# Performance work log

Hardware: AMD Instinct MI355X
Metric: run time of the kernel (lower is better)

Reference implementation:

```python
import jax, jax.numpy as jnp
import numpy as np

B, S, D, FF, V, H, M = 4, 512, 768, 3072, 30000, 12, 64
DH = D // H
N_LAYERS = 12  # shared ALBERT layer applied 12 times


def _positional_encoding():
    pos = jnp.arange(S, dtype=jnp.float32)[:, None]                      # [S,1]
    denom = jnp.power(10000.0, 2.0 * jnp.arange(D, dtype=jnp.float32) / D)
    pe = pos / denom                                                     # [S,D]
    pe = pe.at[1:, 0::2].set(jnp.sin(pe[1:, 0::2]))
    pe = pe.at[1:, 1::2].set(jnp.cos(pe[1:, 1::2]))
    return pe


def setup_inputs() -> dict:
    key = jax.random.key(0)
    ks = jax.random.split(key, 20)
    tok = jax.random.randint(ks[0], (B, S), 0, V)
    texts_onehot = jax.nn.one_hot(tok, V, dtype=jnp.float32)
    w = lambda k, shp: (jax.random.normal(k, shp, jnp.float32) * 0.02)
    return {
        'texts_onehot': texts_onehot,
        'se_w': w(ks[1], (V, D)), 'se_b': w(ks[2], (D,)),
        'wq': w(ks[3], (D, D)), 'bq': w(ks[4], (D,)),
        'wk': w(ks[5], (D, D)), 'bk': w(ks[6], (D,)),
        'wv': w(ks[7], (D, D)), 'bv': w(ks[8], (D,)),
        'wo': w(ks[9], (D, D)), 'bo': w(ks[10], (D,)),
        'w1': w(ks[11], (D, FF)), 'b1': w(ks[12], (FF,)),
        'w2': w(ks[13], (FF, D)), 'b2': w(ks[14], (D,)),
        'we': w(ks[15], (D, V)), 'be': w(ks[16], (V,)),
        'idx': jax.random.randint(ks[17], (B, M), 0, S),
    }


def _layernorm(x):
    mean = jnp.mean(x, axis=-1, keepdims=True)
    var = jnp.mean(jnp.square(x - mean), axis=-1, keepdims=True)
    return (x - mean) / jnp.sqrt(var + 1e-5)


def reference(texts_onehot, se_w, se_b, wq, bq, wk, bk, wv, bv, wo, bo,
              w1, b1, w2, b2, we, be, idx):
    pe = _positional_encoding()                                          # [S,D]
    x = texts_onehot @ se_w + se_b + pe                                  # [B,S,D]
    scale = 1.0 / jnp.sqrt(jnp.float32(DH))

    def mha(x):
        q = (x @ wq + bq).reshape(B, S, H, DH)
        k = (x @ wk + bk).reshape(B, S, H, DH)
        v = (x @ wv + bv).reshape(B, S, H, DH)
        att = jax.nn.softmax(jnp.einsum('bqhd,bkhd->bhqk', q, k) * scale, axis=-1)
        o = jnp.einsum('bhqk,bkhd->bqhd', att, v).reshape(B, S, D)
        return o @ wo + bo

    for _ in range(N_LAYERS):  # same (shared) weights every iteration
        x = _layernorm(x + mha(x))
        x = jax.nn.relu(x @ w1 + b1) @ w2 + b2

    # gather masked positions then project to vocab + log_softmax
    g = jnp.take_along_axis(x, idx[..., None], axis=1)                   # [B,M,D]
    logits = g @ we + be                                                 # [B,M,V]
    return jax.nn.log_softmax(logits, axis=-1).reshape(B * M, V)
```

## Files before the change

### kernel.cpp

```cpp
#include <hip/hip_runtime.h>
#include <hip/hip_bf16.h>
#include <math.h>

#define Bv 4
#define Sv 512
#define Dv 768
#define FFv 3072
#define Vv 30000
#define Vpad 30080
#define Hv 12
#define Mv 64
#define DHv 64
#define NLAYERS 12
#define QKVN 2304

typedef __attribute__((ext_vector_type(8))) short short8;
typedef __attribute__((ext_vector_type(4))) float floatx4;

static __device__ __forceinline__ short f2b(float f) {
  union { float f; unsigned u; } v; v.f = f;
  unsigned r = v.u + 0x7fffu + ((v.u >> 16) & 1u);
  return (short)(r >> 16);
}

#define GLD16(gp, lp) __builtin_amdgcn_global_load_lds( \
    (__attribute__((address_space(1))) void*)(gp), \
    (__attribute__((address_space(3))) void*)(lp), 16, 0, 0)

__global__ __launch_bounds__(256) void transpose_w(
    const float* __restrict__ W, short* __restrict__ Wt,
    int K, int N, int Nout)
{
  __shared__ float t[32][33];
  int n0 = blockIdx.x * 32, k0 = blockIdx.y * 32;
  int tx = threadIdx.x & 31, ty = threadIdx.x >> 5;
  #pragma unroll
  for (int i = 0; i < 4; i++) {
    int k = k0 + ty + i * 8, n = n0 + tx;
    t[ty + i * 8][tx] = (n < N) ? W[(size_t)k * N + n] : 0.f;
  }
  __syncthreads();
  #pragma unroll
  for (int i = 0; i < 4; i++) {
    int n = n0 + ty + i * 8, k = k0 + tx;
    if (n < Nout) Wt[(size_t)n * K + k] = f2b(t[tx][ty + i * 8]);
  }
}

__global__ __launch_bounds__(256) void pack_bias(
    const float* __restrict__ bq, const float* __restrict__ bk,
    const float* __restrict__ bv, float* __restrict__ bqkv)
{
  int i = blockIdx.x * 256 + threadIdx.x;
  if (i < Dv) { bqkv[i] = bq[i]; bqkv[Dv + i] = bk[i]; bqkv[2 * Dv + i] = bv[i]; }
}

__global__ __launch_bounds__(256) void embed_kernel(
    const float* __restrict__ oh, const float* __restrict__ sew,
    const float* __restrict__ seb, float* __restrict__ xf,
    short* __restrict__ xb)
{
  int bs = blockIdx.x;
  int s = bs & (Sv - 1);
  __shared__ int tokS;
  const float* row = oh + (size_t)bs * Vv;
  for (int j = threadIdx.x * 4; j < Vv; j += 256 * 4) {
    float4 f = *(const float4*)(row + j);
    if (f.x != 0.f) tokS = j;
    if (f.y != 0.f) tokS = j + 1;
    if (f.z != 0.f) tokS = j + 2;
    if (f.w != 0.f) tokS = j + 3;
  }
  __syncthreads();
  int tok = tokS;
  for (int d = threadIdx.x; d < Dv; d += 256) {
    float pe = 0.f;
    if (s > 0) {
      float denom = expf(9.210340371976184f * (2.f * (float)d / 768.f));
      float raw = (float)s / denom;
      pe = (d & 1) ? cosf(raw) : sinf(raw);
    }
    float val = sew[(size_t)tok * Dv + d] + seb[d] + pe;
    xf[(size_t)bs * Dv + d] = val;
    xb[(size_t)bs * Dv + d] = f2b(val);
  }
}

template <int BM, int BN, int WM, int WN, int BK>
__global__ __launch_bounds__(256) void gemm_bt(
    const short* __restrict__ A, const short* __restrict__ Bt,
    const float* __restrict__ bias, float* __restrict__ Cf,
    short* __restrict__ Cb, int M, int N, int K, int relu)
{
  constexpr int CPR = BK / 8;
  constexpr int ITA = BM * BK / 2048;
  constexpr int ITB = BN * BK / 2048;
  constexpr int ITMAX = ITA > ITB ? ITA : ITB;
  __shared__ __align__(16) short As[BM * BK];
  __shared__ __align__(16) short Bs[BN * BK];

  int nwgx = gridDim.x;
  int nwg = nwgx * gridDim.y;
  int fid = blockIdx.y * nwgx + blockIdx.x;
  if ((nwg & 7) == 0) fid = (fid & 7) * (nwg >> 3) + (fid >> 3);
  int n0 = (fid % nwgx) * BN, m0 = (fid / nwgx) * BM;

  int tid = threadIdx.x;
  int wave = tid >> 6, lane = tid & 63, quad = lane >> 4, l16 = lane & 15;
  int wm = (wave >> 1) * WM, wn = (wave & 1) * WN;

  floatx4 acc[WM / 16][WN / 16];
  #pragma unroll
  for (int i = 0; i < WM / 16; i++)
    #pragma unroll
    for (int j = 0; j < WN / 16; j++) acc[i][j] = (floatx4){0.f, 0.f, 0.f, 0.f};

  int srow[ITMAX], skc[ITMAX];
  #pragma unroll
  for (int it = 0; it < ITMAX; it++) {
    int c = it * 256 + tid;
    srow[it] = c / CPR;
    skc[it] = (c & (CPR - 1)) ^ (srow[it] & 7);
  }

  for (int k0 = 0; k0 < K; k0 += BK) {
    __syncthreads();
    #pragma unroll
    for (int it = 0; it < ITA; it++)
      GLD16(A + (size_t)(m0 + srow[it]) * K + k0 + skc[it] * 8,
            As + (it * 2048 + wave * 512));
    #pragma unroll
    for (int it = 0; it < ITB; it++)
      GLD16(Bt + (size_t)(n0 + srow[it]) * K + k0 + skc[it] * 8,
            Bs + (it * 2048 + wave * 512));
    __syncthreads();
    #pragma unroll
    for (int kh = 0; kh < BK / 32; kh++) {
      short8 af[WM / 16], bfr[WN / 16];
      int kc = kh * 4 + quad;
      #pragma unroll
      for (int i = 0; i < WM / 16; i++) {
        int ra = wm + i * 16 + l16;
        af[i] = *(const short8*)(As + (ra * CPR + (kc ^ (ra & 7))) * 8);
      }
      #pragma unroll
      for (int j = 0; j < WN / 16; j++) {
        int rb = wn + j * 16 + l16;
        bfr[j] = *(const short8*)(Bs + (rb * CPR + (kc ^ (rb & 7))) * 8);
      }
      #pragma unroll
      for (int i = 0; i < WM / 16; i++)
        #pragma unroll
        for (int j = 0; j < WN / 16; j++)
          acc[i][j] = __builtin_amdgcn_mfma_f32_16x16x32_bf16(af[i], bfr[j], acc[i][j], 0, 0, 0);
    }
  }

  #pragma unroll
  for (int i = 0; i < WM / 16; i++) {
    int row = m0 + wm + i * 16 + quad * 4;
    #pragma unroll
    for (int j = 0; j < WN / 16; j++) {
      int col = n0 + wn + j * 16 + l16;
      if (col < N) {
        float bb = bias ? bias[col] : 0.f;
        #pragma unroll
        for (int r = 0; r < 4; r++) {
          float val = acc[i][j][r] + bb;
          if (relu) val = fmaxf(val, 0.f);
          size_t off = (size_t)(row + r) * N + col;
          if (Cf) Cf[off] = val;
          if (Cb) Cb[off] = f2b(val);
        }
      }
    }
  }
}

__global__ __launch_bounds__(256) void attn_fused(
    const short* __restrict__ qkv, short* __restrict__ O)
{
  __shared__ __align__(16) short lv[64 * 512];
  __shared__ __align__(16) short pbuf[4][16][40];

  int fid = blockIdx.y * gridDim.x + blockIdx.x;
  fid = (fid & 7) * 48 + (fid >> 3);
  int q0 = (fid & 7) * 64;
  int bh = fid >> 3;
  int b = bh / Hv, h = bh - b * Hv;
  int tid = threadIdx.x;
  int wave = tid >> 6, lane = tid & 63, quad = lane >> 4, l16 = lane & 15;

  floatx4 acc[32];
  #pragma unroll
  for (int c = 0; c < 32; c++) acc[c] = (floatx4){0.f, 0.f, 0.f, 0.f};

  const short* Qrow = qkv + (size_t)(b * Sv + q0 + wave * 16 + l16) * QKVN + h * DHv;
  short8 a0 = *(const short8*)(Qrow + quad * 8);
  short8 a1 = *(const short8*)(Qrow + 32 + quad * 8);
  const short* Kbase = qkv + Dv + (size_t)(b * Sv + l16) * QKVN + h * DHv + quad * 8;
  const short* Vbase = qkv + 2 * Dv + h * DHv + (size_t)(b * Sv) * QKVN;

  int kb_t = tid >> 5;
  int n2_t = (tid & 31) * 2;
  short2 vreg[16];

#define LOADQ(qi) do { \
    _Pragma("unroll") \
    for (int i = 0; i < 16; i++) { \
      int kk = (qi) * 128 + i * 8 + kb_t; \
      vreg[i] = *(const short2*)(Vbase + (size_t)kk * QKVN + n2_t); \
    } } while (0)
#define WRITEQ(qi) do { \
    _Pragma("unroll") \
    for (int i = 0; i < 16; i++) { \
      int ch = (qi) * 16 + i; \
      int sw0 = (ch & ~7) | ((ch ^ n2_t) & 7); \
      lv[n2_t * 512 + sw0 * 8 + kb_t] = vreg[i].x; \
      lv[(n2_t + 1) * 512 + (sw0 ^ 1) * 8 + kb_t] = vreg[i].y; \
    } } while (0)

  #pragma unroll
  for (int g = 0; g < 4; g++) {
    if (g > 0) WRITEQ(g - 1);
    LOADQ(g);
    #pragma unroll
    for (int cc = 0; cc < 8; cc++) {
      int c = g * 8 + cc;
      const short* Kp = Kbase + (size_t)c * 16 * QKVN;
      short8 b0 = *(const short8*)(Kp);
      short8 b1 = *(const short8*)(Kp + 32);
      acc[c] = __builtin_amdgcn_mfma_f32_16x16x32_bf16(a0, b0, acc[c], 0, 0, 0);
      acc[c] = __builtin_amdgcn_mfma_f32_16x16x32_bf16(a1, b1, acc[c], 0, 0, 0);
    }
  }

  float inv[4];
  #pragma unroll
  for (int r = 0; r < 4; r++) {
    float m = -1e30f;
    #pragma unroll
    for (int c = 0; c < 32; c++) m = fmaxf(m, acc[c][r]);
    m = fmaxf(m, __shfl_xor(m, 1));
    m = fmaxf(m, __shfl_xor(m, 2));
    m = fmaxf(m, __shfl_xor(m, 4));
    m = fmaxf(m, __shfl_xor(m, 8));
    float s = 0.f;
    #pragma unroll
    for (int c = 0; c < 32; c++) {
      float e = __expf((acc[c][r] - m) * 0.125f);
      acc[c][r] = e; s += e;
    }
    s += __shfl_xor(s, 1);
    s += __shfl_xor(s, 2);
    s += __shfl_xor(s, 4);
    s += __shfl_xor(s, 8);
    inv[r] = 1.f / s;
  }

  WRITEQ(3);
  __syncthreads();

  floatx4 acc_o[4];
  #pragma unroll
  for (int j = 0; j < 4; j++) acc_o[j] = (floatx4){0.f, 0.f, 0.f, 0.f};

  #pragma unroll
  for (int kc = 0; kc < 16; kc++) {
    #pragma unroll
    for (int half = 0; half < 2; half++) {
      int c = 2 * kc + half;
      #pragma unroll
      for (int r = 0; r < 4; r++)
        pbuf[wave][quad * 4 + r][half * 16 + l16] = f2b(acc[c][r] * inv[r]);
    }
    short8 af = *(const short8*)(&pbuf[wave][l16][quad * 8]);
    #pragma unroll
    for (int j = 0; j < 4; j++) {
      int n = j * 16 + l16;
      int ch = kc * 4 + quad;
      int sw = (ch & ~7) | ((ch ^ n) & 7);
      short8 bf = *(const short8*)(lv + n * 512 + sw * 8);
      acc_o[j] = __builtin_amdgcn_mfma_f32_16x16x32_bf16(af, bf, acc_o[j], 0, 0, 0);
    }
  }
#undef LOADQ
#undef WRITEQ

  int row = q0 + wave * 16 + quad * 4;
  #pragma unroll
  for (int j = 0; j < 4; j++) {
    int col = h * DHv + j * 16 + l16;
    #pragma unroll
    for (int r = 0; r < 4; r++)
      O[(size_t)(b * Sv + row + r) * Dv + col] = f2b(acc_o[j][r]);
  }
}

__global__ __launch_bounds__(256) void addln_kernel(
    float* __restrict__ xf, const float* __restrict__ mh,
    short* __restrict__ xb)
{
  int r = blockIdx.x, t = threadIdx.x;
  size_t base = (size_t)r * Dv;
  float v[3];
  #pragma unroll
  for (int i = 0; i < 3; i++) {
    int d = t + i * 256;
    v[i] = xf[base + d] + mh[base + d];
  }
  __shared__ float red[256];
  red[t] = v[0] + v[1] + v[2];
  __syncthreads();
  for (int s2 = 128; s2 > 0; s2 >>= 1) { if (t < s2) red[t] += red[t + s2]; __syncthreads(); }
  float mean = red[0] * (1.f / 768.f);
  __syncthreads();
  float sq = 0.f;
  #pragma unroll
  for (int i = 0; i < 3; i++) { float d2 = v[i] - mean; sq += d2 * d2; }
  red[t] = sq;
  __syncthreads();
  for (int s2 = 128; s2 > 0; s2 >>= 1) { if (t < s2) red[t] += red[t + s2]; __syncthreads(); }
  float inv = rsqrtf(red[0] * (1.f / 768.f) + 1e-5f);
  #pragma unroll
  for (int i = 0; i < 3; i++) {
    int d = t + i * 256;
    float o = (v[i] - mean) * inv;
    xf[base + d] = o;
    xb[base + d] = f2b(o);
  }
}

__global__ __launch_bounds__(256) void gather_kernel(
    const short* __restrict__ xb, const int* __restrict__ idx,
    short* __restrict__ g)
{
  int bm = blockIdx.x;
  int b = bm >> 6;
  int s = idx[bm];
  for (int d = threadIdx.x; d < Dv; d += 256)
    g[(size_t)bm * Dv + d] = xb[(size_t)(b * Sv + s) * Dv + d];
}

__global__ __launch_bounds__(256) void lsm_kernel(
    const float* __restrict__ L, float* __restrict__ out)
{
  int r = blockIdx.x, t = threadIdx.x;
  const float* p = L + (size_t)r * Vv;
  float m = -1e30f;
  for (int j = t; j < Vv; j += 256) m = fmaxf(m, p[j]);
  __shared__ float red[256];
  red[t] = m;
  __syncthreads();
  for (int s2 = 128; s2 > 0; s2 >>= 1) { if (t < s2) red[t] = fmaxf(red[t], red[t + s2]); __syncthreads(); }
  m = red[0];
  __syncthreads();
  float s = 0.f;
  for (int j = t; j < Vv; j += 256) s += expf(p[j] - m);
  red[t] = s;
  __syncthreads();
  for (int s2 = 128; s2 > 0; s2 >>= 1) { if (t < s2) red[t] += red[t + s2]; __syncthreads(); }
  float lse = m + logf(red[0]);
  for (int j = t; j < Vv; j += 256) out[(size_t)r * Vv + j] = p[j] - lse;
}

extern "C" void kernel_launch(void* const* d_in, const int* in_sizes, int n_in,
                              void* d_out, int out_size, void* d_ws, size_t ws_size,
                              hipStream_t stream) {
  const float* oh  = (const float*)d_in[0];
  const float* sew = (const float*)d_in[1];
  const float* seb = (const float*)d_in[2];
  const float* wq  = (const float*)d_in[3];  const float* bq = (const float*)d_in[4];
  const float* wk  = (const float*)d_in[5];  const float* bk = (const float*)d_in[6];
  const float* wv  = (const float*)d_in[7];  const float* bv = (const float*)d_in[8];
  const float* wo  = (const float*)d_in[9];  const float* bo = (const float*)d_in[10];
  const float* w1  = (const float*)d_in[11]; const float* b1 = (const float*)d_in[12];
  const float* w2  = (const float*)d_in[13]; const float* b2 = (const float*)d_in[14];
  const float* we  = (const float*)d_in[15]; const float* be = (const float*)d_in[16];
  const int*   idx = (const int*)d_in[17];
  float* out = (float*)d_out;

  char* p = (char*)d_ws;
  auto alloc = [&](size_t bytes) -> char* {
    char* r = p; p += (bytes + 255) & ~(size_t)255; return r;
  };
  const size_t BS = (size_t)Bv * Sv;
  short* wqkv_t = (short*)alloc((size_t)QKVN * Dv * 2);
  short* wo_t   = (short*)alloc((size_t)Dv * Dv * 2);
  short* w1_t   = (short*)alloc((size_t)FFv * Dv * 2);
  short* w2_t   = (short*)alloc((size_t)Dv * FFv * 2);
  float* bqkv   = (float*)alloc(QKVN * 4);
  short* xb     = (short*)alloc(BS * Dv * 2);
  float* xf     = (float*)alloc(BS * Dv * 4);
  short* g      = (short*)alloc((size_t)Bv * Mv * Dv * 2);
  char*  TR     = p;
  short* qkv   = (short*)TR;
  short* o     = (short*)(TR + ((BS * QKVN * 2 + 255) & ~(size_t)255));
  float* mh    = (float*)((char*)o + ((BS * Dv * 2 + 255) & ~(size_t)255));
  short* t1    = (short*)((char*)mh + ((BS * Dv * 4 + 255) & ~(size_t)255));
  short* we_t = (short*)TR;
  float* lg   = (float*)(TR + (((size_t)Vpad * Dv * 2 + 255) & ~(size_t)255));

  transpose_w<<<dim3(24, 24), 256, 0, stream>>>(wq, wqkv_t,            Dv, Dv, Dv);
  transpose_w<<<dim3(24, 24), 256, 0, stream>>>(wk, wqkv_t + Dv * Dv,  Dv, Dv, Dv);
  transpose_w<<<dim3(24, 24), 256, 0, stream>>>(wv, wqkv_t + 2*Dv*Dv,  Dv, Dv, Dv);
  transpose_w<<<dim3(24, 24), 256, 0, stream>>>(wo, wo_t,              Dv, Dv, Dv);
  transpose_w<<<dim3(96, 24), 256, 0, stream>>>(w1, w1_t,              Dv, FFv, FFv);
  transpose_w<<<dim3(24, 96), 256, 0, stream>>>(w2, w2_t,              FFv, Dv, Dv);
  pack_bias<<<3, 256, 0, stream>>>(bq, bk, bv, bqkv);

  embed_kernel<<<(int)BS, 256, 0, stream>>>(oh, sew, seb, xf, xb);

  dim3 gQKV(QKVN / 128, (int)BS / 128);
  dim3 gD64(Dv / 64, (int)BS / 64);
  dim3 gFF(FFv / 128, (int)BS / 128);
  for (int l = 0; l < NLAYERS; l++) {
    gemm_bt<128,128,64,64,64><<<gQKV, 256, 0, stream>>>(xb, wqkv_t, bqkv, nullptr, qkv, (int)BS, QKVN, Dv, 0);
    attn_fused<<<dim3(Sv / 64, Bv * Hv), 256, 0, stream>>>(qkv, o);
    gemm_bt<64,64,32,32,128><<<gD64, 256, 0, stream>>>(o, wo_t, bo, mh, nullptr, (int)BS, Dv, Dv, 0);
    addln_kernel<<<(int)BS, 256, 0, stream>>>(xf, mh, xb);
    gemm_bt<128,128,64,64,64><<<gFF, 256, 0, stream>>>(xb, w1_t, b1, nullptr, t1, (int)BS, FFv, Dv, 1);
    gemm_bt<64,64,32,32,128><<<gD64, 256, 0, stream>>>(t1, w2_t, b2, xf, xb, (int)BS, Dv, FFv, 0);
  }

  transpose_w<<<dim3(940, 24), 256, 0, stream>>>(we, we_t, Dv, Vv, Vpad);
  gather_kernel<<<Bv * Mv, 256, 0, stream>>>(xb, idx, g);
  gemm_bt<128,128,64,64,64><<<dim3(Vpad / 128, (Bv * Mv) / 128), 256, 0, stream>>>(
      g, we_t, be, lg, nullptr, Bv * Mv, Vv, Dv, 0);
  lsm_kernel<<<Bv * Mv, 256, 0, stream>>>(lg, out);
}
```

Baseline: 2.055 ms.

## Double-buffer GEMM tiles, fuse vocab weight conversion, and vectorize LN/log-softmax

The bf16 GEMM now double-buffers its LDS tiles, so the global-to-LDS copy of the next K tile runs while MFMAs consume the current one, with a vmcnt wait plus barrier between steps. The vocab projection no longer transposes the 30000x768 fp32 weight up front. A new GEMM reads the fp32 weight directly and converts it to bf16 into LDS on the fly. Add+LayerNorm switches to one wave per row with float4 loads and shuffle reductions, and log-softmax uses float4 accesses. The cost is double the LDS in the GEMM, which may lower occupancy, and scalar 2-byte LDS stores in the new vocab GEMM.

```diff
diff --git a/kernel.cpp b/kernel.cpp
--- a/kernel.cpp
+++ b/kernel.cpp
@@ -15,6 +15,7 @@
 #define QKVN 2304
 
 typedef __attribute__((ext_vector_type(8))) short short8;
+typedef __attribute__((ext_vector_type(4))) short short4v;
 typedef __attribute__((ext_vector_type(4))) float floatx4;
 
 static __device__ __forceinline__ short f2b(float f) {
@@ -26,6 +27,11 @@
 #define GLD16(gp, lp) __builtin_amdgcn_global_load_lds( \
     (__attribute__((address_space(1))) void*)(gp), \
     (__attribute__((address_space(3))) void*)(lp), 16, 0, 0)
+
+#define VMCNT0_BARRIER() do { \
+    asm volatile("s_waitcnt vmcnt(0)" ::: "memory"); \
+    __builtin_amdgcn_s_barrier(); \
+  } while (0)
 
 __global__ __launch_bounds__(256) void transpose_w(
     const float* __restrict__ W, short* __restrict__ Wt,
@@ -96,8 +102,8 @@
   constexpr int ITA = BM * BK / 2048;
   constexpr int ITB = BN * BK / 2048;
   constexpr int ITMAX = ITA > ITB ? ITA : ITB;
-  __shared__ __align__(16) short As[BM * BK];
-  __shared__ __align__(16) short Bs[BN * BK];
+  __shared__ __align__(16) short As[2][BM * BK];
+  __shared__ __align__(16) short Bs[2][BN * BK];
 
   int nwgx = gridDim.x;
   int nwg = nwgx * gridDim.y;
@@ -123,17 +129,23 @@
     skc[it] = (c & (CPR - 1)) ^ (srow[it] & 7);
   }
 
-  for (int k0 = 0; k0 < K; k0 += BK) {
-    __syncthreads();
+  auto stage = [&](int buf, int k0) {
     #pragma unroll
     for (int it = 0; it < ITA; it++)
       GLD16(A + (size_t)(m0 + srow[it]) * K + k0 + skc[it] * 8,
-            As + (it * 2048 + wave * 512));
+            &As[buf][it * 2048 + wave * 512]);
     #pragma unroll
     for (int it = 0; it < ITB; it++)
       GLD16(Bt + (size_t)(n0 + srow[it]) * K + k0 + skc[it] * 8,
-            Bs + (it * 2048 + wave * 512));
-    __syncthreads();
+            &Bs[buf][it * 2048 + wave * 512]);
+  };
+
+  int nt = K / BK;
+  stage(0, 0);
+  VMCNT0_BARRIER();
+  int cur = 0;
+  for (int t = 0; t < nt; t++) {
+    if (t + 1 < nt) stage(cur ^ 1, (t + 1) * BK);
     #pragma unroll
     for (int kh = 0; kh < BK / 32; kh++) {
       short8 af[WM / 16], bfr[WN / 16];
@@ -141,12 +153,12 @@
       #pragma unroll
       for (int i = 0; i < WM / 16; i++) {
         int ra = wm + i * 16 + l16;
-        af[i] = *(const short8*)(As + (ra * CPR + (kc ^ (ra & 7))) * 8);
+        af[i] = *(const short8*)(&As[cur][(ra * CPR + (kc ^ (ra & 7))) * 8]);
       }
       #pragma unroll
       for (int j = 0; j < WN / 16; j++) {
         int rb = wn + j * 16 + l16;
-        bfr[j] = *(const short8*)(Bs + (rb * CPR + (kc ^ (rb & 7))) * 8);
+        bfr[j] = *(const short8*)(&Bs[cur][(rb * CPR + (kc ^ (rb & 7))) * 8]);
       }
       #pragma unroll
       for (int i = 0; i < WM / 16; i++)
@@ -154,6 +166,8 @@
         for (int j = 0; j < WN / 16; j++)
           acc[i][j] = __builtin_amdgcn_mfma_f32_16x16x32_bf16(af[i], bfr[j], acc[i][j], 0, 0, 0);
     }
+    VMCNT0_BARRIER();
+    cur ^= 1;
   }
 
   #pragma unroll
@@ -172,6 +186,97 @@
           if (Cf) Cf[off] = val;
           if (Cb) Cb[off] = f2b(val);
         }
+      }
+    }
+  }
+}
+
+__global__ __launch_bounds__(256) void gemm_bf32(
+    const short* __restrict__ A, const float* __restrict__ B,
+    const float* __restrict__ bias, float* __restrict__ Cf,
+    int M, int N, int K)
+{
+  __shared__ __align__(16) short As[128 * 64];
+  __shared__ __align__(16) short Bs[128 * 64];
+  int n0 = blockIdx.x * 128, m0 = blockIdx.y * 128;
+  int tid = threadIdx.x;
+  int wave = tid >> 6, lane = tid & 63, quad = lane >> 4, l16 = lane & 15;
+  int wm = (wave >> 1) * 64, wn = (wave & 1) * 64;
+
+  floatx4 acc[4][4];
+  #pragma unroll
+  for (int i = 0; i < 4; i++)
+    #pragma unroll
+    for (int j = 0; j < 4; j++) acc[i][j] = (floatx4){0.f, 0.f, 0.f, 0.f};
+
+  int srow[4], skc[4];
+  #pragma unroll
+  for (int it = 0; it < 4; it++) {
+    int c = it * 256 + tid;
+    srow[it] = c >> 3;
+    skc[it] = (c & 7) ^ (srow[it] & 7);
+  }
+  int bk0 = tid >> 5;
+  int bn  = (tid & 31) * 4;
+
+  for (int k0 = 0; k0 < K; k0 += 64) {
+    __syncthreads();
+    #pragma unroll
+    for (int it = 0; it < 4; it++)
+      GLD16(A + (size_t)(m0 + srow[it]) * K + k0 + skc[it] * 8,
+            As + (it * 2048 + wave * 512));
+    #pragma unroll
+    for (int i = 0; i < 8; i++) {
+      int kk = k0 + bk0 + i * 8;
+      int ng = n0 + bn;
+      float4 bv;
+      if (ng + 3 < N) bv = *(const float4*)(B + (size_t)kk * N + ng);
+      else {
+        bv.x = (ng     < N) ? B[(size_t)kk * N + ng]     : 0.f;
+        bv.y = (ng + 1 < N) ? B[(size_t)kk * N + ng + 1] : 0.f;
+        bv.z = (ng + 2 < N) ? B[(size_t)kk * N + ng + 2] : 0.f;
+        bv.w = (ng + 3 < N) ? B[(size_t)kk * N + ng + 3] : 0.f;
+      }
+      int nA = bn,     nB = bn + 1, nC = bn + 2, nD = bn + 3;
+      Bs[nA * 64 + ((i ^ (nA & 7)) << 3) + bk0] = f2b(bv.x);
+      Bs[nB * 64 + ((i ^ (nB & 7)) << 3) + bk0] = f2b(bv.y);
+      Bs[nC * 64 + ((i ^ (nC & 7)) << 3) + bk0] = f2b(bv.z);
+      Bs[nD * 64 + ((i ^ (nD & 7)) << 3) + bk0] = f2b(bv.w);
+    }
+    __syncthreads();
+    #pragma unroll
+    for (int kh = 0; kh < 2; kh++) {
+      short8 af[4], bfr[4];
+      int kc = kh * 4 + quad;
+      #pragma unroll
+      for (int i = 0; i < 4; i++) {
+        int ra = wm + i * 16 + l16;
+        af[i] = *(const short8*)(As + (ra * 8 + (kc ^ (ra & 7))) * 8);
+      }
+      #pragma unroll
+      for (int j = 0; j < 4; j++) {
+        int rb = wn + j * 16 + l16;
+        bfr[j] = *(const short8*)(Bs + (rb * 8 + (kc ^ (rb & 7))) * 8);
+      }
+      #pragma unroll
+      for (int i = 0; i < 4; i++)
+        #pragma unroll
+        for (int j = 0; j < 4; j++)
+          acc[i][j] = __builtin_amdgcn_mfma_f32_16x16x32_bf16(af[i], bfr[j], acc[i][j], 0, 0, 0);
+    }
+  }
+
+  #pragma unroll
+  for (int i = 0; i < 4; i++) {
+    int row = m0 + wm + i * 16 + quad * 4;
+    #pragma unroll
+    for (int j = 0; j < 4; j++) {
+      int col = n0 + wn + j * 16 + l16;
+      if (col < N) {
+        float bb = bias[col];
+        #pragma unroll
+        for (int r = 0; r < 4; r++)
+          Cf[(size_t)(row + r) * N + col] = acc[i][j][r] + bb;
       }
     }
   }
@@ -301,33 +406,42 @@
     float* __restrict__ xf, const float* __restrict__ mh,
     short* __restrict__ xb)
 {
-  int r = blockIdx.x, t = threadIdx.x;
+  int wave = threadIdx.x >> 6, lane = threadIdx.x & 63;
+  int r = blockIdx.x * 4 + wave;
   size_t base = (size_t)r * Dv;
-  float v[3];
+  float4 v[3];
+  float s = 0.f;
   #pragma unroll
   for (int i = 0; i < 3; i++) {
-    int d = t + i * 256;
-    v[i] = xf[base + d] + mh[base + d];
-  }
-  __shared__ float red[256];
-  red[t] = v[0] + v[1] + v[2];
-  __syncthreads();
-  for (int s2 = 128; s2 > 0; s2 >>= 1) { if (t < s2) red[t] += red[t + s2]; __syncthreads(); }
-  float mean = red[0] * (1.f / 768.f);
-  __syncthreads();
-  float sq = 0.f;
-  #pragma unroll
-  for (int i = 0; i < 3; i++) { float d2 = v[i] - mean; sq += d2 * d2; }
-  red[t] = sq;
-  __syncthreads();
-  for (int s2 = 128; s2 > 0; s2 >>= 1) { if (t < s2) red[t] += red[t + s2]; __syncthreads(); }
-  float inv = rsqrtf(red[0] * (1.f / 768.f) + 1e-5f);
+    int j = (lane + i * 64) * 4;
+    float4 a = *(const float4*)(xf + base + j);
+    float4 b = *(const float4*)(mh + base + j);
+    v[i].x = a.x + b.x; v[i].y = a.y + b.y;
+    v[i].z = a.z + b.z; v[i].w = a.w + b.w;
+    s += v[i].x + v[i].y + v[i].z + v[i].w;
+  }
+  #pragma unroll
+  for (int o = 32; o > 0; o >>= 1) s += __shfl_xor(s, o);
+  float mean = s * (1.f / 768.f);
+  float q = 0.f;
   #pragma unroll
   for (int i = 0; i < 3; i++) {
-    int d = t + i * 256;
-    float o = (v[i] - mean) * inv;
-    xf[base + d] = o;
-    xb[base + d] = f2b(o);
+    float dx = v[i].x - mean, dy = v[i].y - mean;
+    float dz = v[i].z - mean, dw = v[i].w - mean;
+    q += dx * dx + dy * dy + dz * dz + dw * dw;
+  }
+  #pragma unroll
+  for (int o = 32; o > 0; o >>= 1) q += __shfl_xor(q, o);
+  float inv = rsqrtf(q * (1.f / 768.f) + 1e-5f);
+  #pragma unroll
+  for (int i = 0; i < 3; i++) {
+    int j = (lane + i * 64) * 4;
+    float4 o4;
+    o4.x = (v[i].x - mean) * inv; o4.y = (v[i].y - mean) * inv;
+    o4.z = (v[i].z - mean) * inv; o4.w = (v[i].w - mean) * inv;
+    *(float4*)(xf + base + j) = o4;
+    short4v b4 = { f2b(o4.x), f2b(o4.y), f2b(o4.z), f2b(o4.w) };
+    *(short4v*)(xb + base + j) = b4;
   }
 }
 
@@ -346,9 +460,12 @@
     const float* __restrict__ L, float* __restrict__ out)
 {
   int r = blockIdx.x, t = threadIdx.x;
-  const float* p = L + (size_t)r * Vv;
+  const float4* p4 = (const float4*)(L + (size_t)r * Vv);
   float m = -1e30f;
-  for (int j = t; j < Vv; j += 256) m = fmaxf(m, p[j]);
+  for (int j = t; j < Vv / 4; j += 256) {
+    float4 f = p4[j];
+    m = fmaxf(m, fmaxf(fmaxf(f.x, f.y), fmaxf(f.z, f.w)));
+  }
   __shared__ float red[256];
   red[t] = m;
   __syncthreads();
@@ -356,12 +473,20 @@
   m = red[0];
   __syncthreads();
   float s = 0.f;
-  for (int j = t; j < Vv; j += 256) s += expf(p[j] - m);
+  for (int j = t; j < Vv / 4; j += 256) {
+    float4 f = p4[j];
+    s += expf(f.x - m) + expf(f.y - m) + expf(f.z - m) + expf(f.w - m);
+  }
   red[t] = s;
   __syncthreads();
   for (int s2 = 128; s2 > 0; s2 >>= 1) { if (t < s2) red[t] += red[t + s2]; __syncthreads(); }
   float lse = m + logf(red[0]);
-  for (int j = t; j < Vv; j += 256) out[(size_t)r * Vv + j] = p[j] - lse;
+  float4* o4 = (float4*)(out + (size_t)r * Vv);
+  for (int j = t; j < Vv / 4; j += 256) {
+    float4 f = p4[j];
+    f.x -= lse; f.y -= lse; f.z -= lse; f.w -= lse;
+    o4[j] = f;
+  }
 }
 
 extern "C" void kernel_launch(void* const* d_in, const int* in_sizes, int n_in,
@@ -398,8 +523,7 @@
   short* o     = (short*)(TR + ((BS * QKVN * 2 + 255) & ~(size_t)255));
   float* mh    = (float*)((char*)o + ((BS * Dv * 2 + 255) & ~(size_t)255));
   short* t1    = (short*)((char*)mh + ((BS * Dv * 4 + 255) & ~(size_t)255));
-  short* we_t = (short*)TR;
-  float* lg   = (float*)(TR + (((size_t)Vpad * Dv * 2 + 255) & ~(size_t)255));
+  float* lg    = (float*)TR;
 
   transpose_w<<<dim3(24, 24), 256, 0, stream>>>(wq, wqkv_t,            Dv, Dv, Dv);
   transpose_w<<<dim3(24, 24), 256, 0, stream>>>(wk, wqkv_t + Dv * Dv,  Dv, Dv, Dv);
@@ -418,14 +542,13 @@
     gemm_bt<128,128,64,64,64><<<gQKV, 256, 0, stream>>>(xb, wqkv_t, bqkv, nullptr, qkv, (int)BS, QKVN, Dv, 0);
     attn_fused<<<dim3(Sv / 64, Bv * Hv), 256, 0, stream>>>(qkv, o);
     gemm_bt<64,64,32,32,128><<<gD64, 256, 0, stream>>>(o, wo_t, bo, mh, nullptr, (int)BS, Dv, Dv, 0);
-    addln_kernel<<<(int)BS, 256, 0, stream>>>(xf, mh, xb);
+    addln_kernel<<<(int)BS / 4, 256, 0, stream>>>(xf, mh, xb);
     gemm_bt<128,128,64,64,64><<<gFF, 256, 0, stream>>>(xb, w1_t, b1, nullptr, t1, (int)BS, FFv, Dv, 1);
     gemm_bt<64,64,32,32,128><<<gD64, 256, 0, stream>>>(t1, w2_t, b2, xf, xb, (int)BS, Dv, FFv, 0);
   }
 
-  transpose_w<<<dim3(940, 24), 256, 0, stream>>>(we, we_t, Dv, Vv, Vpad);
   gather_kernel<<<Bv * Mv, 256, 0, stream>>>(xb, idx, g);
-  gemm_bt<128,128,64,64,64><<<dim3(Vpad / 128, (Bv * Mv) / 128), 256, 0, stream>>>(
-      g, we_t, be, lg, nullptr, Bv * Mv, Vv, Dv, 0);
+  gemm_bf32<<<dim3(Vpad / 128, (Bv * Mv) / 128), 256, 0, stream>>>(
+      g, we, be, lg, Bv * Mv, Vv, Dv);
   lsm_kernel<<<Bv * Mv, 256, 0, stream>>>(lg, out);
 }
```

Result: faster. 1.975 ms (-3.9%).
